# Kernel tuning notes

Measured on AMD Instinct MI355X. Metric: run time of the kernel, lower is better.

## Reference

```python
import jax, jax.numpy as jnp
import numpy as np

SIG = 2048          # signal length (sig_size)
N_SCALES = 64       # widths = arange(1, 65)
PREC = 10           # pywt/ptwt cwt internal wavefun precision
NFFT = 4096         # >= SIG + Lmax - 1 = 2048 + 1025 - 1 = 3072, power of two


def _build_bank():
    """Replicates pywt/ptwt mexh cwt filter construction (static constants)."""
    xg = np.linspace(-8.0, 8.0, 2 ** PREC)  # mexh wavefun domain, 1024 pts
    psi = (2.0 / (np.sqrt(3.0) * np.pi ** 0.25)) * (1.0 - xg ** 2) * np.exp(-xg ** 2 / 2.0)
    step = xg[1] - xg[0]
    int_psi = np.cumsum(psi) * step          # integrated wavelet
    span = xg[-1] - xg[0]                    # 16.0
    kernels, lens = [], []
    for s in range(1, N_SCALES + 1):
        j = np.floor(np.arange(s * span + 1) / (s * step)).astype(np.int64)
        j = j[j < int_psi.size]
        kernels.append(int_psi[j][::-1])     # reversed resampled int_psi
        lens.append(len(j))
    Lmax = max(lens)                          # 1025
    K = np.zeros((N_SCALES, Lmax), np.float32)
    for i, k in enumerate(kernels):
        K[i, : lens[i]] = k
    # trim: coef length = N + L - 2 after diff; d = (L-2)/2; start = floor(d)
    starts = np.array([(L - 2) // 2 for L in lens], np.int64)
    idx = (starts[:, None] + np.arange(SIG)[None, :]).astype(np.int32)  # [S, N]
    return K, idx


def setup_inputs() -> dict:
    key = jax.random.key(0)
    x = jax.random.normal(key, (512, 1, SIG), dtype=jnp.float32)
    K, idx = _build_bank()
    scales_sqrt = jnp.sqrt(jnp.arange(1, N_SCALES + 1, dtype=jnp.float32))
    return {
        "x": x,
        "kernels": jnp.asarray(K),
        "scales_sqrt": scales_sqrt,
        "trim_idx": jnp.asarray(idx),
    }


def reference(x, kernels, scales_sqrt, trim_idx):
    # x: [B, 1, N] -> [B, N]
    sig = jnp.squeeze(x, 1)
    # Batched full convolution of signal with every scale's filter via one FFT.
    Xf = jnp.fft.rfft(sig, NFFT)              # [B, F]
    Kf = jnp.fft.rfft(kernels, NFFT)          # [S, F]
    conv = jnp.fft.irfft(Xf[:, None, :] * Kf[None, :, :], NFFT)  # [B, S, NFFT]
    dconv = jnp.diff(conv, axis=-1)           # [B, S, NFFT-1]
    # per-scale symmetric trim to N samples (pywt coef[floor(d):-ceil(d)])
    trimmed = jnp.take_along_axis(dconv, trim_idx[None, :, :], axis=-1)  # [B, S, N]
    coef = -scales_sqrt[None, :, None] * trimmed
    return coef.astype(jnp.float32)           # [B, 64, 2048]
```

## Files before the change

kernel.cpp:

```cpp
#include <hip/hip_runtime.h>

#define NFFT 4096
#define SIG  2048
#define NSCALES 64
#define LMAX 1025
#define NBATCH 512
#define NT   256

__device__ __forceinline__ int swz(int a) { return a ^ ((a >> 4) & 14); }

__device__ __forceinline__ float2 cmul(float2 a, float2 b) {
    return make_float2(a.x * b.x - a.y * b.y, a.x * b.y + a.y * b.x);
}

#define TW_ENTRIES 340

__global__ void twiddle_init(float4* __restrict__ TQ, float4* __restrict__ TW) {
    int i = blockIdx.x * blockDim.x + threadIdx.x;
    if (i < 1024) {
        float s1, c1, s2, c2;
        sincospif(i / 2048.0f, &s1, &c1);
        sincospif(i / 1024.0f, &s2, &c2);
        TQ[i] = make_float4(c1, s1, c2, s2);
    } else if (i < 1024 + TW_ENTRIES) {
        int idx = i - 1024;
        int L, j;
        if (idx < 256)      { L = 256; j = idx; }
        else if (idx < 320) { L = 64;  j = idx - 256; }
        else if (idx < 336) { L = 16;  j = idx - 320; }
        else                { L = 4;   j = idx - 336; }
        float fL = (float)L, fj = (float)j;
        float s1, c1, s2, c2, s3, c3;
        sincospif(fj / (2.0f * fL), &s1, &c1);
        sincospif(fj / fL, &s2, &c2);
        sincospif(3.0f * fj / (2.0f * fL), &s3, &c3);
        TW[2 * idx]     = make_float4(c1, s1, c2, s2);
        TW[2 * idx + 1] = make_float4(c3, s3, 0.0f, 0.0f);
    }
}

template <int L, int M, int DIR, int NN>
__device__ __forceinline__ void r4_stage(const float2* __restrict__ src,
                                         float2* __restrict__ dst, int tid) {
    const int G = NN / 4;
    #pragma unroll
    for (int g0 = 0; g0 < G; g0 += NT) {
        int g = g0 + tid;
        int k = g & (M - 1);
        int j = g / M;
        float2 a0 = src[swz(g)];
        float2 a1 = src[swz(g + G)];
        float2 a2 = src[swz(g + 2 * G)];
        float2 a3 = src[swz(g + 3 * G)];
        float2 t0 = make_float2(a0.x + a2.x, a0.y + a2.y);
        float2 t1 = make_float2(a0.x - a2.x, a0.y - a2.y);
        float2 t2 = make_float2(a1.x + a3.x, a1.y + a3.y);
        float2 t3 = make_float2(a1.x - a3.x, a1.y - a3.y);
        float2 jt3 = make_float2(-(float)DIR * t3.y, (float)DIR * t3.x);
        float2 b0 = make_float2(t0.x + t2.x, t0.y + t2.y);
        float2 b2 = make_float2(t0.x - t2.x, t0.y - t2.y);
        float2 b1 = make_float2(t1.x + jt3.x, t1.y + jt3.y);
        float2 b3 = make_float2(t1.x - jt3.x, t1.y - jt3.y);
        float sw, cw;
        sincospif((float)DIR * (float)j * (1.0f / (2 * L)), &sw, &cw);
        float2 w1 = make_float2(cw, sw);
        float2 w2 = make_float2(cw * cw - sw * sw, 2.0f * cw * sw);
        float2 w3 = cmul(w1, w2);
        b1 = cmul(b1, w1);
        b2 = cmul(b2, w2);
        b3 = cmul(b3, w3);
        int base = k + 4 * j * M;
        dst[swz(base)]         = b0;
        dst[swz(base + M)]     = b1;
        dst[swz(base + 2 * M)] = b2;
        dst[swz(base + 3 * M)] = b3;
    }
}

template <int L, int M>
__device__ __forceinline__ void r4_stage_itab(const float2* __restrict__ src,
                                              float2* __restrict__ dst,
                                              const float4* __restrict__ tw,
                                              int tid) {
    const int G = 512;
    #pragma unroll
    for (int g0 = 0; g0 < G; g0 += NT) {
        int g = g0 + tid;
        int k = g & (M - 1);
        int j = g / M;
        float2 a0 = src[swz(g)];
        float2 a1 = src[swz(g + G)];
        float2 a2 = src[swz(g + 2 * G)];
        float2 a3 = src[swz(g + 3 * G)];
        float2 t0 = make_float2(a0.x + a2.x, a0.y + a2.y);
        float2 t1 = make_float2(a0.x - a2.x, a0.y - a2.y);
        float2 t2 = make_float2(a1.x + a3.x, a1.y + a3.y);
        float2 t3 = make_float2(a1.x - a3.x, a1.y - a3.y);
        float2 jt3 = make_float2(-t3.y, t3.x);
        float2 b0 = make_float2(t0.x + t2.x, t0.y + t2.y);
        float2 b2 = make_float2(t0.x - t2.x, t0.y - t2.y);
        float2 b1 = make_float2(t1.x + jt3.x, t1.y + jt3.y);
        float2 b3 = make_float2(t1.x - jt3.x, t1.y - jt3.y);
        if (L > 1) {
            float4 wa = tw[2 * j];
            float4 wb = tw[2 * j + 1];
            b1 = cmul(b1, make_float2(wa.x, wa.y));
            b2 = cmul(b2, make_float2(wa.z, wa.w));
            b3 = cmul(b3, make_float2(wb.x, wb.y));
        }
        int base = k + 4 * j * M;
        dst[swz(base)]         = b0;
        dst[swz(base + M)]     = b1;
        dst[swz(base + 2 * M)] = b2;
        dst[swz(base + 3 * M)] = b3;
    }
}

__global__ __launch_bounds__(NT, 2) void fwd_fft_x(const float* __restrict__ x,
                                                   float2* __restrict__ Xf) {
    __shared__ float2 bufA[NFFT], bufB[NFFT];
    int tid = threadIdx.x;
    int b = blockIdx.x;
    #pragma unroll
    for (int i0 = 0; i0 < NFFT; i0 += NT) {
        int i = i0 + tid;
        float vr = (i < SIG) ? x[(size_t)b * SIG + i] : 0.0f;
        bufA[swz(i)] = make_float2(vr, 0.0f);
    }
    __syncthreads();
    r4_stage<1024, 1, -1, 4096>(bufA, bufB, tid); __syncthreads();
    r4_stage<256, 4, -1, 4096>(bufB, bufA, tid); __syncthreads();
    r4_stage<64, 16, -1, 4096>(bufA, bufB, tid); __syncthreads();
    r4_stage<16, 64, -1, 4096>(bufB, bufA, tid); __syncthreads();
    r4_stage<4, 256, -1, 4096>(bufA, bufB, tid); __syncthreads();
    r4_stage<1, 1024, -1, 4096>(bufB, bufA, tid); __syncthreads();
    float2* Xrow = Xf + (size_t)b * NFFT;
    #pragma unroll
    for (int i0 = 0; i0 < NFFT; i0 += NT) {
        int i = i0 + tid;
        Xrow[i] = bufA[swz(i)];
    }
}

__global__ __launch_bounds__(NT, 2) void fwd_fft_k(const float* __restrict__ ker,
                                                   const float* __restrict__ ssq,
                                                   float2* __restrict__ Kf) {
    __shared__ float2 bufA[NFFT], bufB[NFFT];
    int tid = threadIdx.x;
    int s = blockIdx.x;
    #pragma unroll
    for (int i0 = 0; i0 < NFFT; i0 += NT) {
        int i = i0 + tid;
        float vr = (i < LMAX) ? ker[(size_t)s * LMAX + i] : 0.0f;
        bufA[swz(i)] = make_float2(vr, 0.0f);
    }
    __syncthreads();
    r4_stage<1024, 1, -1, 4096>(bufA, bufB, tid); __syncthreads();
    r4_stage<256, 4, -1, 4096>(bufB, bufA, tid); __syncthreads();
    r4_stage<64, 16, -1, 4096>(bufA, bufB, tid); __syncthreads();
    r4_stage<16, 64, -1, 4096>(bufB, bufA, tid); __syncthreads();
    r4_stage<4, 256, -1, 4096>(bufA, bufB, tid); __syncthreads();
    r4_stage<1, 1024, -1, 4096>(bufB, bufA, tid); __syncthreads();
    float scale = -ssq[s] * (1.0f / (float)NFFT);
    float2* Krow = Kf + (size_t)s * NFFT;
    #pragma unroll
    for (int i0 = 0; i0 < NFFT; i0 += NT) {
        int i = i0 + tid;
        float sn, cs;
        sincospif((float)i * (1.0f / 2048.0f), &sn, &cs);
        float2 fac = make_float2(scale * (cs - 1.0f), scale * sn);
        Krow[i] = cmul(bufA[swz(i)], fac);
    }
}

__global__ __launch_bounds__(NT, 4) void conv_ifft(const float2* __restrict__ Xf,
                                                   const float2* __restrict__ Kf,
                                                   const int* __restrict__ trim,
                                                   const float4* __restrict__ TQ,
                                                   const float4* __restrict__ TW,
                                                   float* __restrict__ out) {
    __shared__ float2 bufA[2048], bufB[2048];
    int tid = threadIdx.x;
    int b = blockIdx.x >> 6;
    int s = blockIdx.x & 63;
    const float2* X = Xf + (size_t)b * NFFT;
    const float2* K = Kf + (size_t)s * NFFT;

    #pragma unroll
    for (int j0 = 0; j0 < 1024; j0 += NT) {
        int j = j0 + tid;
        float2 P0 = cmul(X[j], K[j]);
        float2 P1 = cmul(X[j + 1024], K[j + 1024]);
        float2 P2 = cmul(X[j + 2048], K[j + 2048]);
        float2 P3 = cmul(X[j + 3072], K[j + 3072]);
        float4 tq = TQ[j];
        float cj = tq.x, sj = tq.y;
        float2 d02 = make_float2(P0.x - P2.x, P0.y - P2.y);
        float2 itd = cmul(make_float2(-sj, cj), d02);
        float2 Qa = make_float2(P0.x + P2.x + itd.x,
                                P0.y + P2.y + itd.y);
        float2 d13 = make_float2(P1.x - P3.x, P1.y - P3.y);
        float2 td = cmul(make_float2(cj, sj), d13);
        float2 Qb = make_float2(P1.x + P3.x - td.x,
                                P1.y + P3.y - td.y);
        float2 u = make_float2(Qa.x + Qb.x, Qa.y + Qb.y);
        float2 dq = make_float2(Qa.x - Qb.x, Qa.y - Qb.y);
        float2 v = cmul(dq, make_float2(tq.z, tq.w));
        int p = swz(2 * j);
        bufA[p] = u;
        bufA[p + 1] = v;
    }
    __syncthreads();
    r4_stage_itab<256, 2>(bufA, bufB, TW, tid);        __syncthreads();
    r4_stage_itab<64, 8>(bufB, bufA, TW + 2 * 256, tid); __syncthreads();
    r4_stage_itab<16, 32>(bufA, bufB, TW + 2 * 320, tid); __syncthreads();
    r4_stage_itab<4, 128>(bufB, bufA, TW + 2 * 336, tid); __syncthreads();
    r4_stage_itab<1, 512>(bufA, bufB, TW, tid);        __syncthreads();

    int start = trim[s * SIG];
    const float* f = (const float*)bufB;
    float* orow = out + (size_t)blockIdx.x * SIG;
    #pragma unroll
    for (int n0 = 0; n0 < SIG; n0 += NT) {
        int n = n0 + tid;
        int t = start + n;
        orow[n] = f[2 * swz(t >> 1) + (t & 1)];
    }
}

extern "C" void kernel_launch(void* const* d_in, const int* in_sizes, int n_in,
                              void* d_out, int out_size, void* d_ws, size_t ws_size,
                              hipStream_t stream) {
    const float* x    = (const float*)d_in[0];
    const float* ker  = (const float*)d_in[1];
    const float* ssq  = (const float*)d_in[2];
    const int*   trim = (const int*)d_in[3];
    float*       out  = (float*)d_out;

    float2* Xf = (float2*)d_ws;
    float2* Kf = Xf + (size_t)NBATCH * NFFT;
    float4* TQ = (float4*)(Kf + (size_t)NSCALES * NFFT);
    float4* TW = TQ + 1024;

    hipLaunchKernelGGL(twiddle_init, dim3(8), dim3(256), 0, stream, TQ, TW);
    hipLaunchKernelGGL(fwd_fft_x, dim3(NBATCH), dim3(NT), 0, stream, x, Xf);
    hipLaunchKernelGGL(fwd_fft_k, dim3(NSCALES), dim3(NT), 0, stream, ker, ssq, Kf);
    hipLaunchKernelGGL(conv_ifft, dim3(NBATCH * NSCALES), dim3(NT), 0, stream,
                       Xf, Kf, trim, TQ, TW, out);
}
```

Measured before the change: 466.6 us.

## Vectorize conv_ifft butterflies with float4 pairs and fuse last stage into output

Reworks the inverse-FFT kernel so each thread processes two adjacent complex points using 128-bit global and LDS accesses in the pointwise multiply/pack and in every radix-4 stage. The final radix-4 stage is fused with the trim/store: only the three output quarters that can fall in the trimmed window are computed, and they are written straight from registers to global memory. This removes the last LDS round trip and barrier. The cost is bounds-checked scalar stores at unaligned offsets and reliance on the swizzle keeping pairs contiguous.

```diff
diff --git a/kernel.cpp b/kernel.cpp
--- a/kernel.cpp
+++ b/kernel.cpp
@@ -11,6 +11,19 @@
 
 __device__ __forceinline__ float2 cmul(float2 a, float2 b) {
     return make_float2(a.x * b.x - a.y * b.y, a.x * b.y + a.y * b.x);
+}
+__device__ __forceinline__ float4 add4(float4 a, float4 b) {
+    return make_float4(a.x + b.x, a.y + b.y, a.z + b.z, a.w + b.w);
+}
+__device__ __forceinline__ float4 sub4(float4 a, float4 b) {
+    return make_float4(a.x - b.x, a.y - b.y, a.z - b.z, a.w - b.w);
+}
+__device__ __forceinline__ float4 mulI4(float4 a) {
+    return make_float4(-a.y, a.x, -a.w, a.z);
+}
+__device__ __forceinline__ float4 cmul4(float4 a, float2 w) {
+    return make_float4(a.x * w.x - a.y * w.y, a.x * w.y + a.y * w.x,
+                       a.z * w.x - a.w * w.y, a.z * w.y + a.w * w.x);
 }
 
 #define TW_ENTRIES 340
@@ -78,42 +91,38 @@
 }
 
 template <int L, int M>
-__device__ __forceinline__ void r4_stage_itab(const float2* __restrict__ src,
-                                              float2* __restrict__ dst,
-                                              const float4* __restrict__ tw,
-                                              int tid) {
-    const int G = 512;
-    #pragma unroll
-    for (int g0 = 0; g0 < G; g0 += NT) {
-        int g = g0 + tid;
-        int k = g & (M - 1);
-        int j = g / M;
-        float2 a0 = src[swz(g)];
-        float2 a1 = src[swz(g + G)];
-        float2 a2 = src[swz(g + 2 * G)];
-        float2 a3 = src[swz(g + 3 * G)];
-        float2 t0 = make_float2(a0.x + a2.x, a0.y + a2.y);
-        float2 t1 = make_float2(a0.x - a2.x, a0.y - a2.y);
-        float2 t2 = make_float2(a1.x + a3.x, a1.y + a3.y);
-        float2 t3 = make_float2(a1.x - a3.x, a1.y - a3.y);
-        float2 jt3 = make_float2(-t3.y, t3.x);
-        float2 b0 = make_float2(t0.x + t2.x, t0.y + t2.y);
-        float2 b2 = make_float2(t0.x - t2.x, t0.y - t2.y);
-        float2 b1 = make_float2(t1.x + jt3.x, t1.y + jt3.y);
-        float2 b3 = make_float2(t1.x - jt3.x, t1.y - jt3.y);
-        if (L > 1) {
-            float4 wa = tw[2 * j];
-            float4 wb = tw[2 * j + 1];
-            b1 = cmul(b1, make_float2(wa.x, wa.y));
-            b2 = cmul(b2, make_float2(wa.z, wa.w));
-            b3 = cmul(b3, make_float2(wb.x, wb.y));
-        }
-        int base = k + 4 * j * M;
-        dst[swz(base)]         = b0;
-        dst[swz(base + M)]     = b1;
-        dst[swz(base + 2 * M)] = b2;
-        dst[swz(base + 3 * M)] = b3;
-    }
+__device__ __forceinline__ void r4i_pair(const float2* __restrict__ src,
+                                         float2* __restrict__ dst,
+                                         const float4* __restrict__ tw,
+                                         int u) {
+    int g = 2 * u;
+    float4 a0 = *(const float4*)&src[swz(g)];
+    float4 a1 = *(const float4*)&src[swz(g + 512)];
+    float4 a2 = *(const float4*)&src[swz(g + 1024)];
+    float4 a3 = *(const float4*)&src[swz(g + 1536)];
+    float4 t0 = add4(a0, a2);
+    float4 t1 = sub4(a0, a2);
+    float4 t2 = add4(a1, a3);
+    float4 t3 = sub4(a1, a3);
+    float4 jt3 = mulI4(t3);
+    float4 b0 = add4(t0, t2);
+    float4 b2 = sub4(t0, t2);
+    float4 b1 = add4(t1, jt3);
+    float4 b3 = sub4(t1, jt3);
+    int j = g / M;
+    int k = g & (M - 1);
+    if (L > 1) {
+        float4 wa = tw[2 * j];
+        float4 wb = tw[2 * j + 1];
+        b1 = cmul4(b1, make_float2(wa.x, wa.y));
+        b2 = cmul4(b2, make_float2(wa.z, wa.w));
+        b3 = cmul4(b3, make_float2(wb.x, wb.y));
+    }
+    int base = k + 4 * j * M;
+    *(float4*)&dst[swz(base)]         = b0;
+    *(float4*)&dst[swz(base + M)]     = b1;
+    *(float4*)&dst[swz(base + 2 * M)] = b2;
+    *(float4*)&dst[swz(base + 3 * M)] = b3;
 }
 
 __global__ __launch_bounds__(NT, 2) void fwd_fft_x(const float* __restrict__ x,
@@ -173,58 +182,99 @@
     }
 }
 
+__device__ __forceinline__ float4 pack_one(float2 X0, float2 X1, float2 X2,
+                                           float2 X3, float2 K0, float2 K1,
+                                           float2 K2, float2 K3, float4 tq) {
+    float2 P0 = cmul(X0, K0);
+    float2 P1 = cmul(X1, K1);
+    float2 P2 = cmul(X2, K2);
+    float2 P3 = cmul(X3, K3);
+    float cj = tq.x, sj = tq.y;
+    float2 d02 = make_float2(P0.x - P2.x, P0.y - P2.y);
+    float2 itd = cmul(make_float2(-sj, cj), d02);
+    float2 Qa = make_float2(P0.x + P2.x + itd.x, P0.y + P2.y + itd.y);
+    float2 d13 = make_float2(P1.x - P3.x, P1.y - P3.y);
+    float2 td = cmul(make_float2(cj, sj), d13);
+    float2 Qb = make_float2(P1.x + P3.x - td.x, P1.y + P3.y - td.y);
+    float2 u = make_float2(Qa.x + Qb.x, Qa.y + Qb.y);
+    float2 dq = make_float2(Qa.x - Qb.x, Qa.y - Qb.y);
+    float2 v = cmul(dq, make_float2(tq.z, tq.w));
+    return make_float4(u.x, u.y, v.x, v.y);
+}
+
 __global__ __launch_bounds__(NT, 4) void conv_ifft(const float2* __restrict__ Xf,
                                                    const float2* __restrict__ Kf,
                                                    const int* __restrict__ trim,
                                                    const float4* __restrict__ TQ,
                                                    const float4* __restrict__ TW,
                                                    float* __restrict__ out) {
-    __shared__ float2 bufA[2048], bufB[2048];
-    int tid = threadIdx.x;
+    __shared__ float4 bufA4[1024], bufB4[1024];
+    float2* bufA = (float2*)bufA4;
+    float2* bufB = (float2*)bufB4;
+    int u = threadIdx.x;
     int b = blockIdx.x >> 6;
     int s = blockIdx.x & 63;
     const float2* X = Xf + (size_t)b * NFFT;
     const float2* K = Kf + (size_t)s * NFFT;
 
     #pragma unroll
-    for (int j0 = 0; j0 < 1024; j0 += NT) {
-        int j = j0 + tid;
-        float2 P0 = cmul(X[j], K[j]);
-        float2 P1 = cmul(X[j + 1024], K[j + 1024]);
-        float2 P2 = cmul(X[j + 2048], K[j + 2048]);
-        float2 P3 = cmul(X[j + 3072], K[j + 3072]);
-        float4 tq = TQ[j];
-        float cj = tq.x, sj = tq.y;
-        float2 d02 = make_float2(P0.x - P2.x, P0.y - P2.y);
-        float2 itd = cmul(make_float2(-sj, cj), d02);
-        float2 Qa = make_float2(P0.x + P2.x + itd.x,
-                                P0.y + P2.y + itd.y);
-        float2 d13 = make_float2(P1.x - P3.x, P1.y - P3.y);
-        float2 td = cmul(make_float2(cj, sj), d13);
-        float2 Qb = make_float2(P1.x + P3.x - td.x,
-                                P1.y + P3.y - td.y);
-        float2 u = make_float2(Qa.x + Qb.x, Qa.y + Qb.y);
-        float2 dq = make_float2(Qa.x - Qb.x, Qa.y - Qb.y);
-        float2 v = cmul(dq, make_float2(tq.z, tq.w));
-        int p = swz(2 * j);
-        bufA[p] = u;
-        bufA[p + 1] = v;
+    for (int v0 = 0; v0 < 512; v0 += NT) {
+        int v = v0 + u;
+        int j = 2 * v;
+        float4 Xa = *(const float4*)&X[j];
+        float4 Xb = *(const float4*)&X[j + 1024];
+        float4 Xc = *(const float4*)&X[j + 2048];
+        float4 Xd = *(const float4*)&X[j + 3072];
+        float4 Ka = *(const float4*)&K[j];
+        float4 Kb = *(const float4*)&K[j + 1024];
+        float4 Kc = *(const float4*)&K[j + 2048];
+        float4 Kd = *(const float4*)&K[j + 3072];
+        float4 r0 = pack_one(make_float2(Xa.x, Xa.y), make_float2(Xb.x, Xb.y),
+                             make_float2(Xc.x, Xc.y), make_float2(Xd.x, Xd.y),
+                             make_float2(Ka.x, Ka.y), make_float2(Kb.x, Kb.y),
+                             make_float2(Kc.x, Kc.y), make_float2(Kd.x, Kd.y),
+                             TQ[j]);
+        float4 r1 = pack_one(make_float2(Xa.z, Xa.w), make_float2(Xb.z, Xb.w),
+                             make_float2(Xc.z, Xc.w), make_float2(Xd.z, Xd.w),
+                             make_float2(Ka.z, Ka.w), make_float2(Kb.z, Kb.w),
+                             make_float2(Kc.z, Kc.w), make_float2(Kd.z, Kd.w),
+                             TQ[j + 1]);
+        *(float4*)&bufA[swz(2 * j)]     = r0;
+        *(float4*)&bufA[swz(2 * j + 2)] = r1;
     }
     __syncthreads();
-    r4_stage_itab<256, 2>(bufA, bufB, TW, tid);        __syncthreads();
-    r4_stage_itab<64, 8>(bufB, bufA, TW + 2 * 256, tid); __syncthreads();
-    r4_stage_itab<16, 32>(bufA, bufB, TW + 2 * 320, tid); __syncthreads();
-    r4_stage_itab<4, 128>(bufB, bufA, TW + 2 * 336, tid); __syncthreads();
-    r4_stage_itab<1, 512>(bufA, bufB, TW, tid);        __syncthreads();
-
-    int start = trim[s * SIG];
-    const float* f = (const float*)bufB;
-    float* orow = out + (size_t)blockIdx.x * SIG;
-    #pragma unroll
-    for (int n0 = 0; n0 < SIG; n0 += NT) {
-        int n = n0 + tid;
-        int t = start + n;
-        orow[n] = f[2 * swz(t >> 1) + (t & 1)];
+    r4i_pair<256, 2>(bufA, bufB, TW, u);           __syncthreads();
+    r4i_pair<64, 8>(bufB, bufA, TW + 2 * 256, u);  __syncthreads();
+    r4i_pair<16, 32>(bufA, bufB, TW + 2 * 320, u); __syncthreads();
+    r4i_pair<4, 128>(bufB, bufA, TW + 2 * 336, u); __syncthreads();
+
+    {
+        int g = 2 * u;
+        float4 a0 = *(const float4*)&bufA[swz(g)];
+        float4 a1 = *(const float4*)&bufA[swz(g + 512)];
+        float4 a2 = *(const float4*)&bufA[swz(g + 1024)];
+        float4 a3 = *(const float4*)&bufA[swz(g + 1536)];
+        float4 t0 = add4(a0, a2);
+        float4 t1 = sub4(a0, a2);
+        float4 t2 = add4(a1, a3);
+        float4 t3 = sub4(a1, a3);
+        float4 jt3 = mulI4(t3);
+        float4 b0 = add4(t0, t2);
+        float4 b1 = add4(t1, jt3);
+        float4 b2 = sub4(t0, t2);
+        int start = trim[s * SIG];
+        float* orow = out + (size_t)blockIdx.x * SIG;
+        float4 rs[3] = {b0, b1, b2};
+        #pragma unroll
+        for (int r = 0; r < 3; ++r) {
+            int o = 4 * u + 1024 * r - start;
+            float vals[4] = {rs[r].x, rs[r].y, rs[r].z, rs[r].w};
+            #pragma unroll
+            for (int e = 0; e < 4; ++e) {
+                int n = o + e;
+                if ((unsigned)n < (unsigned)SIG) orow[n] = vals[e];
+            }
+        }
     }
 }
 
```

Result: no change. 461.3 us (-1.1%).
